# Optimization experiments

Measured on AMD Instinct MI355X. Metric: run time of the kernel, lower is better.

Reference implementation:

```python
import jax, jax.numpy as jnp
import numpy as np

B, L, C = 2, 2048, 1024
DK, H = 64, 16

def setup_inputs() -> dict:
    key = jax.random.key(0)
    ks = jax.random.split(key, 12)
    def lin(kw, kb, out_dim, in_dim):
        w = jax.random.normal(kw, (out_dim, in_dim), jnp.float32) * (1.0 / np.sqrt(in_dim))
        b = jnp.zeros((out_dim,), jnp.float32)
        return w, b
    WQ_w, WQ_b = lin(ks[0], ks[1], DK * H, C)
    WK_w, WK_b = lin(ks[2], ks[3], DK * H, C)
    WV_w, WV_b = lin(ks[4], ks[5], DK * H, C)
    WO_w, WO_b = lin(ks[6], ks[7], C, DK * H)
    qx = jax.random.normal(ks[8], (B, L, C), jnp.float32)
    kx = jax.random.normal(ks[9], (B, L, C), jnp.float32)
    vx = jax.random.normal(ks[10], (B, L, C), jnp.float32)
    maskPAD = jax.random.randint(ks[11], (B, L, L), 0, 2, jnp.int32)
    return {"qx": qx, "kx": kx, "vx": vx, "maskPAD": maskPAD,
            "WQ_w": WQ_w, "WQ_b": WQ_b, "WK_w": WK_w, "WK_b": WK_b,
            "WV_w": WV_w, "WV_b": WV_b, "WO_w": WO_w, "WO_b": WO_b}

def reference(qx, kx, vx, maskPAD, WQ_w, WQ_b, WK_w, WK_b, WV_w, WV_b, WO_w, WO_b):
    Bq, qL, _ = qx.shape
    kvL = kx.shape[1]
    # projections -> [B, H, L, DK]
    q = (qx @ WQ_w.T + WQ_b).reshape(Bq, qL, H, DK).transpose(0, 2, 1, 3)
    k = (kx @ WK_w.T + WK_b).reshape(Bq, kvL, H, DK).transpose(0, 2, 1, 3)
    v = (vx @ WV_w.T + WV_b).reshape(Bq, kvL, H, DK).transpose(0, 2, 1, 3)
    scores = jnp.einsum('bhqd,bhkd->bhqk', q, k) / np.sqrt(DK).astype(np.float32)
    scores = jnp.where((maskPAD == 0)[:, None, :, :], jnp.float32(-2**15 + 1), scores)
    alpha = jax.nn.softmax(scores, axis=3)  # dropout p=0 (eval)
    z = jnp.einsum('bhqk,bhkd->bhqd', alpha, v)
    z = z.transpose(0, 2, 1, 3).reshape(Bq, qL, H * DK)
    return z @ WO_w.T + WO_b
```

## Files before the change

### kernel.cpp

```cpp
#include <hip/hip_runtime.h>
#include <hip/hip_bf16.h>
#include <stdint.h>
#include <math.h>

typedef short short8 __attribute__((ext_vector_type(8)));
typedef short short4v __attribute__((ext_vector_type(4)));
typedef float float4v __attribute__((ext_vector_type(4)));
typedef float float2v __attribute__((ext_vector_type(2)));

static __device__ __forceinline__ float bf2f(uint16_t u) {
    union { uint32_t i; float f; } x; x.i = ((uint32_t)u) << 16; return x.f;
}
static __device__ __forceinline__ uint16_t f2bf(float f) {
    union { float f; uint32_t i; } x; x.f = f;
    uint32_t u = x.i;
    u += 0x7FFFu + ((u >> 16) & 1u);
    return (uint16_t)(u >> 16);
}
static __device__ __forceinline__ uint16_t f2bf_hw(float f) {
    __hip_bfloat16 h = __float2bfloat16(f);
    uint16_t u; __builtin_memcpy(&u, &h, 2); return u;
}
static __device__ __forceinline__ uint16_t f2bf_sane(float f) {
    uint16_t u = f2bf(f);
    if ((u & 0x7F80u) == 0x7F80u) u = 0;
    return u;
}
static __device__ __forceinline__ float san_f32(float f) {
    union { float f; uint32_t i; } x; x.f = f;
    if (((x.i >> 23) & 0xFFu) == 0xFFu) return 0.f;
    return x.f;
}
static __device__ __forceinline__ void gll16(const void* g, void* l) {
    __builtin_amdgcn_global_load_lds((const __attribute__((address_space(1))) void*)g,
                                     (__attribute__((address_space(3))) void*)l,
                                     16, 0, 0);
}
static __device__ __forceinline__ short8 load8(const void* p, size_t off, int fp32) {
    if (!fp32) return *(const short8*)((const uint16_t*)p + off);
    const float* f = (const float*)p + off;
    const float4v a = *(const float4v*)f;
    const float4v b = *(const float4v*)(f + 4);
    short8 r;
    r[0] = (short)f2bf(a[0]); r[1] = (short)f2bf(a[1]);
    r[2] = (short)f2bf(a[2]); r[3] = (short)f2bf(a[3]);
    r[4] = (short)f2bf(b[0]); r[5] = (short)f2bf(b[1]);
    r[6] = (short)f2bf(b[2]); r[7] = (short)f2bf(b[3]);
    return r;
}

static __device__ __forceinline__ float fexp2(float x) {
#if __has_builtin(__builtin_amdgcn_exp2f)
    return __builtin_amdgcn_exp2f(x);
#else
    float r; asm("v_exp_f32 %0, %1\ns_nop 0" : "=v"(r) : "v"(x)); return r;
#endif
}

static __device__ __forceinline__ float maskexp2(float s, uint32_t nib, int r) {
    union { float f; uint32_t u; } x; x.f = s;
    const uint32_t keep = (uint32_t)(((int32_t)(nib << (31 - r))) >> 31);
    x.u = (x.u & keep) | (~keep & 0xFF800000u);
    return fexp2(x.f);
}

static __device__ __forceinline__ float4v mfma16_bf16(short4v a, short4v b, float4v c) {
#if __has_builtin(__builtin_amdgcn_mfma_f32_16x16x16bf16_1k)
    return __builtin_amdgcn_mfma_f32_16x16x16bf16_1k(a, b, c, 0, 0, 0);
#else
    float4v d = c;
    asm volatile("v_mfma_f32_16x16x16_bf16 %0, %1, %2, %0"
                 : "+v"(d) : "v"(a), "v"(b));
    return d;
#endif
}

__global__ __launch_bounds__(256) void pack_kernel(
    const int* __restrict__ mask, uint64_t* __restrict__ mask64,
    const uint16_t* __restrict__ qx, int* __restrict__ flag,
    const void* wq, const void* wk, const void* wv, const void* wo,
    const void* bq, const void* bk, const void* bv, const void* bo,
    uint16_t* __restrict__ cW, uint16_t* __restrict__ cB)
{
    const int bx = blockIdx.x;
    const int tid = threadIdx.x;
    if (bx < 1024) {
        const int wave = tid >> 6, lane = tid & 63;
        const int row = bx * 4 + wave;
        const int* src = mask + (size_t)row * 2048;
#pragma unroll 4
        for (int j = 0; j < 32; ++j) {
            const int m = src[j * 64 + lane];
            const uint64_t bal = __ballot(m != 0);
            if (lane == 0) mask64[(size_t)row * 32 + j] = bal;
        }
        return;
    }
    __shared__ int s;
    if (tid == 0) s = 0;
    __syncthreads();
    int bad = 0;
#pragma unroll 8
    for (int i = 0; i < 64; ++i) {
        const uint16_t u = qx[tid * 64 + i];
        bad |= ((u & 0x7F80u) == 0x7F80u) ? 1 : 0;
    }
    if (bad) atomicOr(&s, 1);
    __syncthreads();
    const int mode = s;
    if (bx == 1024) {
        if (tid == 0) *flag = mode;
        return;
    }
    if (!mode) return;
    if (bx < 1537) {
        const int idx8 = (bx - 1025) * 256 + tid;
#pragma unroll
        for (int t = 0; t < 4; ++t) {
            const void* src = (t == 0) ? wq : (t == 1) ? wk : (t == 2) ? wv : wo;
            *(short8*)(cW + (size_t)t * 1048576 + (size_t)idx8 * 8) =
                load8(src, (size_t)idx8 * 8, 1);
        }
    } else {
        if (tid < 128) {
#pragma unroll
            for (int t = 0; t < 4; ++t) {
                const void* src = (t == 0) ? bq : (t == 1) ? bk : (t == 2) ? bv : bo;
                *(short8*)(cB + t * 1024 + tid * 8) = load8(src, (size_t)tid * 8, 1);
            }
        }
    }
}

template <int MI, int NI>
static __device__ __forceinline__ void gemm_tile(
    const void* __restrict__ A, int afp32,
    const uint16_t* __restrict__ W,
    const uint16_t* __restrict__ bias, void* __restrict__ C,
    int c_fp32, float out_scale, int bx, int by)
{
    constexpr int TM = MI * 32, TN = NI * 32;
    constexpr int GA = (TM / 16) / 4;
    __shared__ __align__(16) uint16_t sA[TM * 32];
    __shared__ __align__(16) uint16_t sB[TN * 32];

    const int tid  = threadIdx.x;
    const int wave = tid >> 6;
    const int lane = tid & 63;
    const int quad = lane >> 4;
    const int l15  = lane & 15;
    const int m0 = by * TM;
    const int n0 = bx * TN;
    const int wm = (wave >> 1) * (MI * 16);
    const int wn = (wave & 1) * (NI * 16);
    const int r16 = lane >> 2;
    const int ch  = lane & 3;

    float4v acc[MI][NI] = {};
    float4v pa[GA][2];
    const float* Af = (const float*)A;

    if (afp32) {
#pragma unroll
        for (int gi = 0; gi < GA; ++gi) {
            const int g = wave + gi * 4;
            const float* p = Af + (size_t)(m0 + g * 16 + r16) * 1024 + ch * 8;
            pa[gi][0] = *(const float4v*)p;
            pa[gi][1] = *(const float4v*)(p + 4);
        }
    }

    for (int k0 = 0; k0 < 1024; k0 += 32) {
        __syncthreads();
        if (afp32) {
#pragma unroll
            for (int gi = 0; gi < GA; ++gi) {
                const int g = wave + gi * 4;
                short8 r;
                r[0] = (short)f2bf_hw(pa[gi][0][0]);
                r[1] = (short)f2bf_hw(pa[gi][0][1]);
                r[2] = (short)f2bf_hw(pa[gi][0][2]);
                r[3] = (short)f2bf_hw(pa[gi][0][3]);
                r[4] = (short)f2bf_hw(pa[gi][1][0]);
                r[5] = (short)f2bf_hw(pa[gi][1][1]);
                r[6] = (short)f2bf_hw(pa[gi][1][2]);
                r[7] = (short)f2bf_hw(pa[gi][1][3]);
                *(short8*)((char*)sA + (size_t)g * 1024 + (size_t)lane * 16) = r;
            }
        } else {
            const uint16_t* Ah = (const uint16_t*)A;
#pragma unroll
            for (int g = wave; g < TM / 16; g += 4)
                gll16(Ah + (size_t)(m0 + g * 16 + r16) * 1024 + k0 + ch * 8,
                      (char*)sA + (size_t)g * 1024);
        }
#pragma unroll
        for (int g = wave; g < TN / 16; g += 4)
            gll16(W + (size_t)(n0 + g * 16 + r16) * 1024 + k0 + ch * 8,
                  (char*)sB + (size_t)g * 1024);
        asm volatile("s_waitcnt vmcnt(0)" ::: "memory");
        __syncthreads();

        if (afp32 && k0 + 32 < 1024) {
#pragma unroll
            for (int gi = 0; gi < GA; ++gi) {
                const int g = wave + gi * 4;
                const float* p = Af + (size_t)(m0 + g * 16 + r16) * 1024 + (k0 + 32) + ch * 8;
                pa[gi][0] = *(const float4v*)p;
                pa[gi][1] = *(const float4v*)(p + 4);
            }
        }

        short8 af[MI], bfr[NI];
#pragma unroll
        for (int i = 0; i < MI; ++i)
            af[i] = *(const short8*)&sA[(wm + i * 16 + l15) * 32 + quad * 8];
#pragma unroll
        for (int j = 0; j < NI; ++j)
            bfr[j] = *(const short8*)&sB[(wn + j * 16 + l15) * 32 + quad * 8];
#pragma unroll
        for (int mi = 0; mi < MI; ++mi)
#pragma unroll
            for (int ni = 0; ni < NI; ++ni)
                acc[mi][ni] = __builtin_amdgcn_mfma_f32_16x16x32_bf16(
                    af[mi], bfr[ni], acc[mi][ni], 0, 0, 0);
    }

#pragma unroll
    for (int ni = 0; ni < NI; ++ni) {
        const int n = n0 + wn + ni * 16 + l15;
        const float bv = bf2f(bias[n]);
#pragma unroll
        for (int mi = 0; mi < MI; ++mi) {
            const int mbase = m0 + wm + mi * 16 + quad * 4;
#pragma unroll
            for (int r = 0; r < 4; ++r) {
                const float v = (acc[mi][ni][r] + bv) * out_scale;
                const size_t idx = (size_t)(mbase + r) * 1024 + n;
                if (c_fp32) ((float*)C)[idx] = san_f32(v);
                else        ((uint16_t*)C)[idx] = f2bf_sane(v);
            }
        }
    }
}

__global__ __launch_bounds__(256) void qkv_kernel(
    const void* qxr, const void* kxr, const void* vxr,
    const uint16_t* rwq, const uint16_t* rwk, const uint16_t* rwv,
    const uint16_t* rbq, const uint16_t* rbk, const uint16_t* rbv,
    const uint16_t* cW, const uint16_t* cB,
    uint16_t* Q, uint16_t* K, uint16_t* V, const int* flag)
{
    const int mode = *flag;
    const int wgid = blockIdx.x + (blockIdx.y << 3) + (blockIdx.z << 8);
    const int xcd = wgid & 7;
    const int s   = wgid >> 3;
    const int panel = xcd * 12 + (s >> 3);
    const int bx = s & 7;
    const int z  = panel >> 5;
    const int by = panel & 31;

    const void* A = (z == 0) ? qxr : (z == 1) ? kxr : vxr;
    const uint16_t* W = mode ? cW + (size_t)z * 1048576
                             : ((z == 0) ? rwq : (z == 1) ? rwk : rwv);
    const uint16_t* b = mode ? cB + z * 1024
                             : ((z == 0) ? rbq : (z == 1) ? rbk : rbv);
    uint16_t* C = (z == 0) ? Q : (z == 1) ? K : V;
    const float sc = (z == 0) ? 0.18033688f : 1.0f;
    gemm_tile<4, 4>(A, mode, W, b, C, 0, sc, bx, by);
}

__global__ __launch_bounds__(256) void out_kernel(
    const uint16_t* Z, const uint16_t* rwo, const uint16_t* rbo,
    const uint16_t* cW, const uint16_t* cB, void* out, const int* flag)
{
    const int mode = *flag;
    const uint16_t* W = mode ? cW + 3 * 1048576 : rwo;
    const uint16_t* b = mode ? cB + 3 * 1024 : rbo;
    const int wgid = blockIdx.x + (blockIdx.y << 3);
    const int xcd = wgid & 7;
    const int s   = wgid >> 3;
    const int by  = xcd * 8 + (s >> 3);
    const int bx  = s & 7;
    gemm_tile<2, 4>(Z, 0, W, b, out, mode, 1.0f, bx, by);
}

__global__ __launch_bounds__(256) void vtrans_kernel(
    const uint16_t* __restrict__ Vp, uint16_t* __restrict__ Vt)
{
    __shared__ __align__(16) uint16_t t[64][72];
    const int tid = threadIdx.x;
    const int lt = blockIdx.x, h = blockIdx.y, b = blockIdx.z;
#pragma unroll
    for (int p = 0; p < 2; ++p) {
        const int r = p * 32 + (tid >> 3);
        const int c = (tid & 7) * 8;
        *(short8*)&t[r][c] =
            *(const short8*)(Vp + (size_t)(b * 2048 + lt * 64 + r) * 1024 + h * 64 + c);
    }
    __syncthreads();
#pragma unroll
    for (int p = 0; p < 2; ++p) {
        const int d = p * 32 + (tid >> 3);
        const int c = (tid & 7) * 8;
        short8 v;
#pragma unroll
        for (int j = 0; j < 8; ++j) v[j] = (short)t[c + j][d];
        *(short8*)(Vt + (size_t)((b * 16 + h) * 64 + d) * 2048 + lt * 64 + c) = v;
    }
}

#define VS 72

__global__ __launch_bounds__(256, 4) void attn_kernel(
    const uint16_t* __restrict__ Q, const uint16_t* __restrict__ Kp,
    const uint16_t* __restrict__ Vt, const uint64_t* __restrict__ mask64,
    uint16_t* __restrict__ Oa, uint16_t* __restrict__ Ob,
    uint16_t* __restrict__ Oc, float* __restrict__ lpart)
{
    __shared__ __align__(16) uint16_t sK[64 * VS];
    __shared__ __align__(16) uint16_t sV[64 * VS];

    const int tid = threadIdx.x;
    const int wave = tid >> 6, lane = tid & 63;
    const int quad = lane >> 4, l15 = lane & 15;
    const int qt = blockIdx.x, h = blockIdx.y;
    const int b = blockIdx.z & 1, seg = blockIdx.z >> 1;
    const int q0 = qt * 128;
    const int qw = q0 + wave * 32;

    const int srow = tid >> 2;
    const int sc0  = tid & 3;

    short8 qf[2][2];
#pragma unroll
    for (int mi = 0; mi < 2; ++mi)
#pragma unroll
        for (int kk = 0; kk < 2; ++kk)
            qf[mi][kk] = *(const short8*)(Q + (size_t)(b * 2048 + qw + mi * 16 + l15) * 1024
                                            + h * 64 + (quad + 4 * kk) * 8);

    const uint64_t* mrow[2];
#pragma unroll
    for (int mj = 0; mj < 2; ++mj)
        mrow[mj] = mask64 + (size_t)(b * 2048 + qw + mj * 16 + l15) * 32;

    const uint16_t* Kbase = Kp + (size_t)(b * 2048 + srow) * 1024 + h * 64;
    const uint16_t* Vbase = Vt + (size_t)((b * 16 + h) * 64 + srow) * 2048;

    float4v oaccT[4][2] = {};
    float2v lsum2[2] = {};

    const int kt_lo = seg * 11;
    const int kt_hi = (seg == 2) ? 32 : kt_lo + 11;

    short8 kx0 = *(const short8*)(Kbase + (size_t)(kt_lo * 64) * 1024 + sc0 * 8);
    short8 kx1 = *(const short8*)(Kbase + (size_t)(kt_lo * 64) * 1024 + (sc0 + 4) * 8);
    short8 vx0 = *(const short8*)(Vbase + kt_lo * 64 + sc0 * 8);
    short8 vx1 = *(const short8*)(Vbase + kt_lo * 64 + (sc0 + 4) * 8);

    for (int kt = kt_lo; kt < kt_hi; ++kt) {
        const uint64_t mwq0 = mrow[0][kt] >> (quad * 4);
        const uint64_t mwq1 = mrow[1][kt] >> (quad * 4);
        __syncthreads();
        *(short8*)&sK[srow * VS + sc0 * 8]       = kx0;
        *(short8*)&sK[srow * VS + (sc0 + 4) * 8] = kx1;
        *(short8*)&sV[srow * VS + sc0 * 8]       = vx0;
        *(short8*)&sV[srow * VS + (sc0 + 4) * 8] = vx1;
        __syncthreads();

        short8 nk0, nk1, nv0, nv1;
        if (kt + 1 < kt_hi) {
            const int k0n = (kt + 1) * 64;
            nk0 = *(const short8*)(Kbase + (size_t)k0n * 1024 + sc0 * 8);
            nk1 = *(const short8*)(Kbase + (size_t)k0n * 1024 + (sc0 + 4) * 8);
            nv0 = *(const short8*)(Vbase + k0n + sc0 * 8);
            nv1 = *(const short8*)(Vbase + k0n + (sc0 + 4) * 8);
        } else {
            nk0 = kx0; nk1 = kx1; nv0 = vx0; nv1 = vx1;
        }

        float4v sacc[2][4] = {};
        __builtin_amdgcn_s_setprio(1);
#pragma unroll
        for (int ni = 0; ni < 4; ++ni) {
            const int row = ni * 16 + l15;
#pragma unroll
            for (int kk = 0; kk < 2; ++kk) {
                const short8 kf = *(const short8*)&sK[row * VS + (quad + 4 * kk) * 8];
                sacc[0][ni] = __builtin_amdgcn_mfma_f32_16x16x32_bf16(kf, qf[0][kk], sacc[0][ni], 0, 0, 0);
                sacc[1][ni] = __builtin_amdgcn_mfma_f32_16x16x32_bf16(kf, qf[1][kk], sacc[1][ni], 0, 0, 0);
            }
        }
        __builtin_amdgcn_s_setprio(0);

        short4v pf[2][4];
#pragma unroll
        for (int mj = 0; mj < 2; ++mj) {
            const uint64_t mwq = mj ? mwq1 : mwq0;
#pragma unroll
            for (int ni = 0; ni < 4; ++ni) {
                const uint32_t nib = (uint32_t)(mwq >> (ni * 16)) & 0xFu;
                const float p0 = maskexp2(sacc[mj][ni][0], nib, 0);
                const float p1 = maskexp2(sacc[mj][ni][1], nib, 1);
                const float p2 = maskexp2(sacc[mj][ni][2], nib, 2);
                const float p3 = maskexp2(sacc[mj][ni][3], nib, 3);
                float2v lo; lo[0] = p0; lo[1] = p1;
                float2v hi; hi[0] = p2; hi[1] = p3;
                lsum2[mj] += lo;
                lsum2[mj] += hi;
                short4v t;
                t[0] = (short)f2bf_hw(p0);
                t[1] = (short)f2bf_hw(p1);
                t[2] = (short)f2bf_hw(p2);
                t[3] = (short)f2bf_hw(p3);
                pf[mj][ni] = t;
            }
        }

        __builtin_amdgcn_s_setprio(1);
#pragma unroll
        for (int di = 0; di < 4; ++di) {
            const int row = di * 16 + l15;
#pragma unroll
            for (int ni = 0; ni < 4; ++ni) {
                const short4v vf = *(const short4v*)&sV[row * VS + ni * 16 + quad * 4];
                oaccT[di][0] = mfma16_bf16(vf, pf[0][ni], oaccT[di][0]);
                oaccT[di][1] = mfma16_bf16(vf, pf[1][ni], oaccT[di][1]);
            }
        }
        __builtin_amdgcn_s_setprio(0);

        kx0 = nk0; kx1 = nk1; vx0 = nv0; vx1 = nv1;
    }

#if !__has_builtin(__builtin_amdgcn_mfma_f32_16x16x16bf16_1k)
    asm volatile("s_nop 7\ns_nop 7\ns_nop 7" ::: "memory");
#endif

    float lsum[2];
#pragma unroll
    for (int mj = 0; mj < 2; ++mj) lsum[mj] = lsum2[mj][0] + lsum2[mj][1];

#pragma unroll
    for (int mj = 0; mj < 2; ++mj) {
        lsum[mj] += __shfl_xor(lsum[mj], 16);
        lsum[mj] += __shfl_xor(lsum[mj], 32);
    }

    uint16_t* Op = (seg == 0) ? Oa : (seg == 1) ? Ob : Oc;
#pragma unroll
    for (int mj = 0; mj < 2; ++mj) {
        const int qrow = qw + mj * 16 + l15;
#pragma unroll
        for (int di = 0; di < 4; ++di) {
            short4v o;
#pragma unroll
            for (int r = 0; r < 4; ++r) o[r] = (short)f2bf_hw(oaccT[di][mj][r]);
            *(short4v*)(Op + (size_t)(b * 2048 + qrow) * 1024 + h * 64 + di * 16 + quad * 4) = o;
        }
        if (quad == 0)
            lpart[seg * 65536 + (b * 16 + h) * 2048 + qrow] = lsum[mj];
    }
}

__global__ __launch_bounds__(256) void combine_kernel(
    const uint16_t* __restrict__ Oa, const uint16_t* __restrict__ Ob,
    const uint16_t* __restrict__ Oc, const float* __restrict__ lpart,
    uint16_t* __restrict__ Z)
{
    const int e8 = blockIdx.x * 256 + threadIdx.x;
    const int flat = e8 * 8;
    const int bh_row = flat >> 10;
    const int h = (flat >> 6) & 15;
    const int b = bh_row >> 11;
    const int row = bh_row & 2047;
    const int lidx = (b * 16 + h) * 2048 + row;
    const float inv = 1.0f / fmaxf(lpart[lidx] + lpart[65536 + lidx] + lpart[131072 + lidx], 1e-37f);
    const short8 a = *(const short8*)(Oa + flat);
    const short8 c = *(const short8*)(Ob + flat);
    const short8 d = *(const short8*)(Oc + flat);
    short8 o;
#pragma unroll
    for (int j = 0; j < 8; ++j)
        o[j] = (short)f2bf_sane((bf2f((uint16_t)a[j]) + bf2f((uint16_t)c[j]) + bf2f((uint16_t)d[j])) * inv);
    *(short8*)(Z + flat) = o;
}

extern "C" void kernel_launch(void* const* d_in, const int* in_sizes, int n_in,
                              void* d_out, int out_size, void* d_ws, size_t ws_size,
                              hipStream_t stream)
{
    const void* qx  = d_in[0];
    const void* kx  = d_in[1];
    const void* vx  = d_in[2];
    const int*  msk = (const int*)d_in[3];

    char* ws = (char*)d_ws;
    const size_t MB = 1024 * 1024;
    uint16_t* cW  = (uint16_t*)(ws + 24 * MB);
    uint16_t* cB  = (uint16_t*)(ws + 32 * MB);
    int*      flg = (int*)(ws + 32 * MB + 16 * 1024);
    uint16_t* Qb  = (uint16_t*)(ws + 33 * MB);
    uint16_t* Kb  = (uint16_t*)(ws + 41 * MB);
    uint16_t* Vb  = (uint16_t*)(ws + 49 * MB);
    uint64_t* m64 = (uint64_t*)(ws + 57 * MB);
    uint16_t* Vt  = (uint16_t*)(ws + 8 * MB);
    uint16_t* Oa  = (uint16_t*)(ws);
    uint16_t* Ob  = (uint16_t*)(ws + 16 * MB);
    uint16_t* Oc  = (uint16_t*)(ws + 49 * MB);
    float*    lp  = (float*)(ws + 24 * MB);
    uint16_t* Zb  = Oa;

    pack_kernel<<<1538, 256, 0, stream>>>(
        msk, m64, (const uint16_t*)qx, flg,
        d_in[4], d_in[6], d_in[8], d_in[10],
        d_in[5], d_in[7], d_in[9], d_in[11], cW, cB);
    qkv_kernel<<<dim3(8, 32, 3), 256, 0, stream>>>(
        qx, kx, vx,
        (const uint16_t*)d_in[4], (const uint16_t*)d_in[6], (const uint16_t*)d_in[8],
        (const uint16_t*)d_in[5], (const uint16_t*)d_in[7], (const uint16_t*)d_in[9],
        cW, cB, Qb, Kb, Vb, flg);
    vtrans_kernel<<<dim3(32, 16, 2), 256, 0, stream>>>(Vb, Vt);
    attn_kernel<<<dim3(16, 16, 6), 256, 0, stream>>>(Qb, Kb, Vt, m64, Oa, Ob, Oc, lp);
    combine_kernel<<<4096, 256, 0, stream>>>(Oa, Ob, Oc, lp, Zb);
    out_kernel<<<dim3(8, 64), 256, 0, stream>>>(
        Zb, (const uint16_t*)d_in[10], (const uint16_t*)d_in[11], cW, cB, d_out, flg);
}
```

Measured before the change: 292.6 us.

## Fuse V transpose into QKV GEMM epilogue and drop separate transpose kernel

The V projection tile now writes its output already transposed, staging it through a padded shared-memory buffer in two halves, so the separate vtrans kernel and its extra read and write of V are removed. Shared buffers move from gemm_tile into the kernels so the transpose staging buffer can be allocated. The attention kernel also changes how threads map to K/V rows when loading into shared memory. In exchange, the QKV kernel uses more LDS and adds two barriers per half in the V epilogue.

```diff
diff --git a/kernel.cpp b/kernel.cpp
--- a/kernel.cpp
+++ b/kernel.cpp
@@ -132,17 +132,19 @@
     }
 }
 
+#define ST_STRIDE 136
+
 template <int MI, int NI>
 static __device__ __forceinline__ void gemm_tile(
+    uint16_t* __restrict__ sA, uint16_t* __restrict__ sB,
+    uint16_t* __restrict__ sT,
     const void* __restrict__ A, int afp32,
     const uint16_t* __restrict__ W,
     const uint16_t* __restrict__ bias, void* __restrict__ C,
-    int c_fp32, float out_scale, int bx, int by)
+    int c_fp32, float out_scale, int bx, int by, int vt)
 {
     constexpr int TM = MI * 32, TN = NI * 32;
     constexpr int GA = (TM / 16) / 4;
-    __shared__ __align__(16) uint16_t sA[TM * 32];
-    __shared__ __align__(16) uint16_t sB[TN * 32];
 
     const int tid  = threadIdx.x;
     const int wave = tid >> 6;
@@ -226,6 +228,44 @@
                     af[mi], bfr[ni], acc[mi][ni], 0, 0, 0);
     }
 
+    if (vt) {
+        const int bb = m0 >> 11;
+        const int l0 = m0 & 2047;
+        const int h2 = n0 >> 6;
+#pragma unroll
+        for (int half = 0; half < 2; ++half) {
+            __syncthreads();
+            if ((wave & 1) == half) {
+#pragma unroll
+                for (int ni = 0; ni < NI; ++ni) {
+                    const int n = n0 + wn + ni * 16 + l15;
+                    const float bv = bf2f(bias[n]);
+                    const int nloc = ni * 16 + l15;
+#pragma unroll
+                    for (int mi = 0; mi < MI; ++mi) {
+                        const int mloc = wm + mi * 16 + quad * 4;
+#pragma unroll
+                        for (int rp = 0; rp < 2; ++rp) {
+                            const uint32_t u =
+                                (uint32_t)f2bf_sane(acc[mi][ni][rp * 2]     + bv) |
+                                ((uint32_t)f2bf_sane(acc[mi][ni][rp * 2 + 1] + bv) << 16);
+                            *(uint32_t*)(sT + nloc * ST_STRIDE + mloc + rp * 2) = u;
+                        }
+                    }
+                }
+            }
+            __syncthreads();
+            const int nrow = tid >> 2, seg = tid & 3;
+            uint16_t* dst = (uint16_t*)C
+                + ((size_t)((bb * 16 + h2 + half) * 64 + nrow)) * 2048 + l0 + seg * 32;
+            const uint16_t* srcT = sT + nrow * ST_STRIDE + seg * 32;
+#pragma unroll
+            for (int j = 0; j < 4; ++j)
+                *(short8*)(dst + j * 8) = *(const short8*)(srcT + j * 8);
+        }
+        return;
+    }
+
 #pragma unroll
     for (int ni = 0; ni < NI; ++ni) {
         const int n = n0 + wn + ni * 16 + l15;
@@ -249,8 +289,12 @@
     const uint16_t* rwq, const uint16_t* rwk, const uint16_t* rwv,
     const uint16_t* rbq, const uint16_t* rbk, const uint16_t* rbv,
     const uint16_t* cW, const uint16_t* cB,
-    uint16_t* Q, uint16_t* K, uint16_t* V, const int* flag)
-{
+    uint16_t* Q, uint16_t* K, uint16_t* Vt, const int* flag)
+{
+    __shared__ __align__(16) uint16_t sA[128 * 32];
+    __shared__ __align__(16) uint16_t sB[128 * 32];
+    __shared__ __align__(16) uint16_t sT[64 * ST_STRIDE];
+
     const int mode = *flag;
     const int wgid = blockIdx.x + (blockIdx.y << 3) + (blockIdx.z << 8);
     const int xcd = wgid & 7;
@@ -265,15 +309,18 @@
                              : ((z == 0) ? rwq : (z == 1) ? rwk : rwv);
     const uint16_t* b = mode ? cB + z * 1024
                              : ((z == 0) ? rbq : (z == 1) ? rbk : rbv);
-    uint16_t* C = (z == 0) ? Q : (z == 1) ? K : V;
+    uint16_t* C = (z == 0) ? Q : (z == 1) ? K : Vt;
     const float sc = (z == 0) ? 0.18033688f : 1.0f;
-    gemm_tile<4, 4>(A, mode, W, b, C, 0, sc, bx, by);
+    gemm_tile<4, 4>(sA, sB, sT, A, mode, W, b, C, 0, sc, bx, by, z == 2);
 }
 
 __global__ __launch_bounds__(256) void out_kernel(
     const uint16_t* Z, const uint16_t* rwo, const uint16_t* rbo,
     const uint16_t* cW, const uint16_t* cB, void* out, const int* flag)
 {
+    __shared__ __align__(16) uint16_t sA[64 * 32];
+    __shared__ __align__(16) uint16_t sB[128 * 32];
+
     const int mode = *flag;
     const uint16_t* W = mode ? cW + 3 * 1048576 : rwo;
     const uint16_t* b = mode ? cB + 3 * 1024 : rbo;
@@ -282,32 +329,7 @@
     const int s   = wgid >> 3;
     const int by  = xcd * 8 + (s >> 3);
     const int bx  = s & 7;
-    gemm_tile<2, 4>(Z, 0, W, b, out, mode, 1.0f, bx, by);
-}
-
-__global__ __launch_bounds__(256) void vtrans_kernel(
-    const uint16_t* __restrict__ Vp, uint16_t* __restrict__ Vt)
-{
-    __shared__ __align__(16) uint16_t t[64][72];
-    const int tid = threadIdx.x;
-    const int lt = blockIdx.x, h = blockIdx.y, b = blockIdx.z;
-#pragma unroll
-    for (int p = 0; p < 2; ++p) {
-        const int r = p * 32 + (tid >> 3);
-        const int c = (tid & 7) * 8;
-        *(short8*)&t[r][c] =
-            *(const short8*)(Vp + (size_t)(b * 2048 + lt * 64 + r) * 1024 + h * 64 + c);
-    }
-    __syncthreads();
-#pragma unroll
-    for (int p = 0; p < 2; ++p) {
-        const int d = p * 32 + (tid >> 3);
-        const int c = (tid & 7) * 8;
-        short8 v;
-#pragma unroll
-        for (int j = 0; j < 8; ++j) v[j] = (short)t[c + j][d];
-        *(short8*)(Vt + (size_t)((b * 16 + h) * 64 + d) * 2048 + lt * 64 + c) = v;
-    }
+    gemm_tile<2, 4>(sA, sB, (uint16_t*)nullptr, Z, 0, W, b, out, mode, 1.0f, bx, by, 0);
 }
 
 #define VS 72
@@ -329,8 +351,8 @@
     const int q0 = qt * 128;
     const int qw = q0 + wave * 32;
 
-    const int srow = tid >> 2;
-    const int sc0  = tid & 3;
+    const int srow = (wave << 4) + l15;
+    const int sc0  = quad;
 
     short8 qf[2][2];
 #pragma unroll
@@ -503,7 +525,6 @@
     int*      flg = (int*)(ws + 32 * MB + 16 * 1024);
     uint16_t* Qb  = (uint16_t*)(ws + 33 * MB);
     uint16_t* Kb  = (uint16_t*)(ws + 41 * MB);
-    uint16_t* Vb  = (uint16_t*)(ws + 49 * MB);
     uint64_t* m64 = (uint64_t*)(ws + 57 * MB);
     uint16_t* Vt  = (uint16_t*)(ws + 8 * MB);
     uint16_t* Oa  = (uint16_t*)(ws);
@@ -520,8 +541,7 @@
         qx, kx, vx,
         (const uint16_t*)d_in[4], (const uint16_t*)d_in[6], (const uint16_t*)d_in[8],
         (const uint16_t*)d_in[5], (const uint16_t*)d_in[7], (const uint16_t*)d_in[9],
-        cW, cB, Qb, Kb, Vb, flg);
-    vtrans_kernel<<<dim3(32, 16, 2), 256, 0, stream>>>(Vb, Vt);
+        cW, cB, Qb, Kb, Vt, flg);
     attn_kernel<<<dim3(16, 16, 6), 256, 0, stream>>>(Qb, Kb, Vt, m64, Oa, Ob, Oc, lp);
     combine_kernel<<<4096, 256, 0, stream>>>(Oa, Ob, Oc, lp, Zb);
     out_kernel<<<dim3(8, 64), 256, 0, stream>>>(
```

After: 346.9 us. 18.5% more time.
